# Kernel optimization log

Hardware: AMD Instinct MI355X
Metric: run time of the kernel (lower is better)

The kernel has to match this reference:

```python
import jax, jax.numpy as jnp
import numpy as np

B, T, DIM = 4, 1024, 2048
H, KVH = 16, 4
HD = DIM // H          # 128
G = H // KVH           # GQA group size = 4


def setup_inputs() -> dict:
    key = jax.random.key(0)
    ks = jax.random.split(key, 4)
    s = 1.0 / np.sqrt(DIM)
    x = jax.random.normal(ks[0], (B, T, DIM), jnp.float32)
    Wq = jax.random.normal(ks[1], (DIM, DIM), jnp.float32) * s
    Wkv = jax.random.normal(ks[2], (DIM, 2 * KVH * HD), jnp.float32) * s
    Wo = jax.random.normal(ks[3], (DIM, DIM), jnp.float32) * s
    # RoPE tables (theta=10000, half-split / rotate-half convention)
    inv_freq = 1.0 / (10000.0 ** (np.arange(0, HD, 2, dtype=np.float64) / HD))
    freqs = np.outer(np.arange(T, dtype=np.float64), inv_freq)  # [T, HD/2]
    cos = jnp.asarray(np.cos(freqs), jnp.float32)
    sin = jnp.asarray(np.sin(freqs), jnp.float32)
    return {"x": x, "Wq": Wq, "Wkv": Wkv, "Wo": Wo, "cos": cos, "sin": sin}


def _rope(u, cos, sin):
    # u: [B,T,heads,HD]; cos/sin: [T, HD/2]
    u1, u2 = jnp.split(u, 2, axis=-1)
    c = cos[None, :, None, :]
    s = sin[None, :, None, :]
    return jnp.concatenate([u1 * c - u2 * s, u1 * s + u2 * c], axis=-1)


def reference(x, Wq, Wkv, Wo, cos, sin):
    Bs, Ts, C = x.shape
    q = (x @ Wq).reshape(Bs, Ts, H, HD)
    kv = (x @ Wkv).reshape(Bs, Ts, 2, KVH, HD)
    k, v = kv[:, :, 0], kv[:, :, 1]
    q = _rope(q, cos, sin)
    k = _rope(k, cos, sin)
    # GQA without materializing repeated K/V: fold group dim into q
    qg = q.reshape(Bs, Ts, KVH, G, HD)
    scores = jnp.einsum('bqhgd,bkhd->bhgqk', qg, k) / np.float32(np.sqrt(HD))
    causal = jnp.tril(jnp.ones((Ts, Ts), bool))
    neg = jnp.finfo(scores.dtype).min
    scores = jnp.where(causal, scores, neg)
    att = jax.nn.softmax(scores, axis=-1)
    out = jnp.einsum('bhgqk,bkhd->bqhgd', att, v).reshape(Bs, Ts, C)
    return out @ Wo
```

## Files before the change

kernel.cpp:

```cpp
#include <hip/hip_runtime.h>

typedef unsigned short u16;
typedef unsigned int u32;
typedef __bf16 bf16x8 __attribute__((ext_vector_type(8)));
typedef float f32x4 __attribute__((ext_vector_type(4)));

#define BB   4
#define TT   1024
#define CDIM 2048
#define NH   16
#define NKV  4
#define HDIM 128

__device__ __forceinline__ float b2f(u16 u) {
    union { u32 i; float f; } x; x.i = ((u32)u) << 16; return x.f;
}
__device__ __forceinline__ u16 f2b(float f) {
    union { float f; u32 i; } x; x.f = f;
    u32 r = (x.i + 0x7fffu + ((x.i >> 16) & 1u)) >> 16;
    return (u16)r;
}
__device__ __forceinline__ void async16(const void* g, void* l) {
    __builtin_amdgcn_global_load_lds((const __attribute__((address_space(1))) void*)g,
                                     (__attribute__((address_space(3))) void*)l, 16, 0, 0);
}
template<int N> __device__ __forceinline__ void waitvm() {
    static_assert(N >= 0 && N <= 8, "unsupported vmcnt");
    if constexpr (N == 0)      asm volatile("s_waitcnt vmcnt(0)" ::: "memory");
    else if constexpr (N == 1) asm volatile("s_waitcnt vmcnt(1)" ::: "memory");
    else if constexpr (N == 2) asm volatile("s_waitcnt vmcnt(2)" ::: "memory");
    else if constexpr (N == 3) asm volatile("s_waitcnt vmcnt(3)" ::: "memory");
    else if constexpr (N == 4) asm volatile("s_waitcnt vmcnt(4)" ::: "memory");
    else if constexpr (N == 5) asm volatile("s_waitcnt vmcnt(5)" ::: "memory");
    else if constexpr (N == 6) asm volatile("s_waitcnt vmcnt(6)" ::: "memory");
    else if constexpr (N == 7) asm volatile("s_waitcnt vmcnt(7)" ::: "memory");
    else                       asm volatile("s_waitcnt vmcnt(8)" ::: "memory");
}

__device__ __forceinline__ bool wave_is_f32(const u16* xp) {
    u16 v = xp[(threadIdx.x & 63) * 2];
    int e = (v >> 7) & 0xFF;
    bool bad = (v != 0) && (e < 90 || e > 160);
    return __popcll(__ballot(bad)) > 16;
}

__global__ __launch_bounds__(256) void pre_k(const void* __restrict__ x,
                                             const void* __restrict__ Wq,
                                             const void* __restrict__ Wkv,
                                             const void* __restrict__ Wo,
                                             u16* __restrict__ xb,
                                             u16* __restrict__ csb,
                                             u16* __restrict__ snb,
                                             u16* __restrict__ WqkvT,
                                             u16* __restrict__ WoT,
                                             const void* __restrict__ cs,
                                             const void* __restrict__ sn) {
    const bool f32m = wave_is_f32((const u16*)x);
    int bid = blockIdx.x;
    if (bid < 8320) {
        const void* src; u16* dst; int i;
        if (bid < 8192)      { src = x;  dst = xb;  i = bid * 256 + threadIdx.x; }
        else if (bid < 8256) { src = cs; dst = csb; i = (bid - 8192) * 256 + threadIdx.x; }
        else                 { src = sn; dst = snb; i = (bid - 8256) * 256 + threadIdx.x; }
        union { u16 u[4]; ushort4 v; } o;
        if (f32m) {
            float4 f = ((const float4*)src)[i];
            o.u[0] = f2b(f.x); o.u[1] = f2b(f.y); o.u[2] = f2b(f.z); o.u[3] = f2b(f.w);
        } else {
            o.v = ((const ushort4*)src)[i];
        }
        ((ushort4*)dst)[i] = o.v;
        return;
    }
    __shared__ alignas(16) u16 tile[64 * 65];
    int t = bid - 8320;
    const void* W; u16* WT; int rows, cols, bx, by;
    if (t < 1024)      { W = Wq;  WT = WqkvT;                    rows = 2048; cols = 2048; bx = t & 31;  by = t >> 5; }
    else if (t < 1536) { int l = t - 1024; W = Wkv; WT = WqkvT + (long)2048 * 2048; rows = 2048; cols = 1024; bx = l & 15; by = l >> 4; }
    else               { int l = t - 1536; W = Wo;  WT = WoT;  rows = 2048; cols = 2048; bx = l & 31;   by = l >> 5; }
    const int r0 = by * 64, c0 = bx * 64;
#pragma unroll
    for (int i = 0; i < 16; i++) {
        int c = threadIdx.x + i * 256;
        int rr = c >> 6, cc = c & 63;
        long idx = (long)(r0 + rr) * cols + c0 + cc;
        tile[rr * 65 + cc] = f32m ? f2b(((const float*)W)[idx]) : ((const u16*)W)[idx];
    }
    __syncthreads();
#pragma unroll
    for (int i = 0; i < 16; i++) {
        int c = threadIdx.x + i * 256;
        int rr = c >> 6, cc = c & 63;
        WT[(long)(c0 + rr) * rows + r0 + cc] = tile[cc * 65 + rr];
    }
}

template<int BM, int BN>
__global__ __launch_bounds__(512, 2) void gemm_t(const u16* __restrict__ A,
                                                 const u16* __restrict__ Bt,
                                                 void* __restrict__ C,
                                                 int N, int Kd,
                                                 const u16* __restrict__ xprobe) {
    constexpr int MF  = BM / 32;
    constexpr int NF  = BN / 64;
    constexpr int MF0 = MF / 2, MF1 = MF - MF0;
    constexpr int NF0 = (NF + 1) / 2, NF1 = NF - NF0;
    constexpr int NAU = BM / 64;
    constexpr int NBU = BN / 64;
    constexpr int NAL = NAU / 2;
    constexpr int NBL = NBU / 2;

    __shared__ alignas(16) u16 As[2][BM * 64];
    __shared__ alignas(16) u16 Bs[2][BN * 64];

    const bool f32m = (xprobe != nullptr) && wave_is_f32(xprobe);
    const int tid = threadIdx.x;
    const int w = tid >> 6, lane = tid & 63;
    const int wm = w >> 2, wn = w & 3;
    const int l16 = lane & 15, quad = lane >> 4;
    const long arow0 = (long)blockIdx.y * BM;
    const long brow0 = (long)blockIdx.x * BN;
    const int NT = Kd >> 6;

    const int srow = tid >> 3, scp = tid & 7;
    const long gst = (long)srow * Kd + ((scp ^ (srow & 7)) << 3);
    const int cst = tid << 3;

    const u16* Ab = A + arow0 * Kd;
    const u16* Bb = Bt + brow0 * Kd;

    auto stageA = [&](int buf, int t, int u0, int u1) {
#pragma unroll
        for (int u = 0; u < NAU; u++)
            if (u >= u0 && u < u1)
                async16(Ab + (long)u * 64 * Kd + t * 64 + gst, &As[buf][u * 4096 + cst]);
    };
    auto stageB = [&](int buf, int t, int u0, int u1) {
#pragma unroll
        for (int u = 0; u < NBU; u++)
            if (u >= u0 && u < u1)
                async16(Bb + (long)u * 64 * Kd + t * 64 + gst, &Bs[buf][u * 4096 + cst]);
    };

    const int R0a = wm * (BM / 2) + l16, sA = R0a & 7;
    const int R0b = wn * (BN / 4) + l16, sB = R0b & 7;
    int aoff[2], boff[2];
    aoff[0] = R0a * 64 + ((quad ^ sA) << 3);
    aoff[1] = R0a * 64 + (((4 + quad) ^ sA) << 3);
    boff[0] = R0b * 64 + ((quad ^ sB) << 3);
    boff[1] = R0b * 64 + (((4 + quad) ^ sB) << 3);

    f32x4 acc[MF][NF];
#pragma unroll
    for (int i = 0; i < MF; i++)
#pragma unroll
        for (int j = 0; j < NF; j++) acc[i][j] = {0.f, 0.f, 0.f, 0.f};

    stageB(0, 0, 0, NBU);
    stageA(0, 0, 0, NAU);
    stageB(1, 1, 0, NBL);
    waitvm<NBL>();
    __builtin_amdgcn_s_barrier();

#pragma unroll 1
    for (int t = 0; t < NT; ++t) {
        const int cur = t & 1, nxt = cur ^ 1;
        const u16* pA = &As[cur][0];
        const u16* pB = &Bs[cur][0];
        bf16x8 afLo[MF0][2], afHi[MF1][2], bfA[NF0][2], bfB[NF1][2];

#pragma unroll
        for (int ks = 0; ks < 2; ks++) {
#pragma unroll
            for (int mt = 0; mt < MF0; mt++)
                afLo[mt][ks] = *(const bf16x8*)&pA[aoff[ks] + mt * 1024];
#pragma unroll
            for (int nt = 0; nt < NF0; nt++)
                bfA[nt][ks] = *(const bf16x8*)&pB[boff[ks] + nt * 1024];
        }
        if (t + 1 < NT) stageB(nxt, t + 1, NBL, NBU);
        __builtin_amdgcn_s_barrier();
        asm volatile("s_waitcnt lgkmcnt(0)" ::: "memory");
        __builtin_amdgcn_sched_barrier(0);
        __builtin_amdgcn_s_setprio(1);
#pragma unroll
        for (int ks = 0; ks < 2; ks++)
#pragma unroll
            for (int mt = 0; mt < MF0; mt++)
#pragma unroll
                for (int nt = 0; nt < NF0; nt++)
                    acc[mt][nt] = __builtin_amdgcn_mfma_f32_16x16x32_bf16(
                        afLo[mt][ks], bfA[nt][ks], acc[mt][nt], 0, 0, 0);
        __builtin_amdgcn_s_setprio(0);

#pragma unroll
        for (int ks = 0; ks < 2; ks++)
#pragma unroll
            for (int nt = 0; nt < NF1; nt++)
                bfB[nt][ks] = *(const bf16x8*)&pB[boff[ks] + (NF0 + nt) * 1024];
        if (t + 1 < NT) stageA(nxt, t + 1, 0, NAL);
        __builtin_amdgcn_s_barrier();
        asm volatile("s_waitcnt lgkmcnt(0)" ::: "memory");
        __builtin_amdgcn_sched_barrier(0);
        __builtin_amdgcn_s_setprio(1);
#pragma unroll
        for (int ks = 0; ks < 2; ks++)
#pragma unroll
            for (int mt = 0; mt < MF0; mt++)
#pragma unroll
                for (int nt = 0; nt < NF1; nt++)
                    acc[mt][NF0 + nt] = __builtin_amdgcn_mfma_f32_16x16x32_bf16(
                        afLo[mt][ks], bfB[nt][ks], acc[mt][NF0 + nt], 0, 0, 0);
        __builtin_amdgcn_s_setprio(0);

#pragma unroll
        for (int ks = 0; ks < 2; ks++)
#pragma unroll
            for (int mt = 0; mt < MF1; mt++)
                afHi[mt][ks] = *(const bf16x8*)&pA[aoff[ks] + (MF0 + mt) * 1024];
        if (t + 1 < NT) stageA(nxt, t + 1, NAL, NAU);
        __builtin_amdgcn_s_barrier();
        asm volatile("s_waitcnt lgkmcnt(0)" ::: "memory");
        __builtin_amdgcn_sched_barrier(0);
        __builtin_amdgcn_s_setprio(1);
#pragma unroll
        for (int ks = 0; ks < 2; ks++)
#pragma unroll
            for (int mt = 0; mt < MF1; mt++)
#pragma unroll
                for (int nt = 0; nt < NF1; nt++)
                    acc[MF0 + mt][NF0 + nt] = __builtin_amdgcn_mfma_f32_16x16x32_bf16(
                        afHi[mt][ks], bfB[nt][ks], acc[MF0 + mt][NF0 + nt], 0, 0, 0);
        __builtin_amdgcn_s_setprio(0);

        if (t + 1 < NT) {
            asm volatile("s_waitcnt vmcnt(0)" ::: "memory");
            __builtin_amdgcn_s_barrier();
            if (t + 2 < NT) stageB(cur, t + 2, 0, NBL);
        }
        __builtin_amdgcn_sched_barrier(0);
        __builtin_amdgcn_s_setprio(1);
#pragma unroll
        for (int ks = 0; ks < 2; ks++)
#pragma unroll
            for (int mt = 0; mt < MF1; mt++)
#pragma unroll
                for (int nt = 0; nt < NF0; nt++)
                    acc[MF0 + mt][nt] = __builtin_amdgcn_mfma_f32_16x16x32_bf16(
                        afHi[mt][ks], bfA[nt][ks], acc[MF0 + mt][nt], 0, 0, 0);
        __builtin_amdgcn_s_setprio(0);
    }

#pragma unroll
    for (int mt = 0; mt < MF; mt++) {
#pragma unroll
        for (int nt = 0; nt < NF; nt++) {
            long col = brow0 + wn * (BN / 4) + nt * 16 + l16;
#pragma unroll
            for (int r = 0; r < 4; r++) {
                long row = arow0 + wm * (BM / 2) + mt * 16 + quad * 4 + r;
                if (f32m) ((float*)C)[row * N + col] = acc[mt][nt][r];
                else      ((u16*)C)[row * N + col] = f2b(acc[mt][nt][r]);
            }
        }
    }
}

__global__ __launch_bounds__(256) void prep_k(const u16* __restrict__ QKVraw,
                                              const u16* __restrict__ cs,
                                              const u16* __restrict__ sn,
                                              u16* __restrict__ Qr,
                                              u16* __restrict__ Kr,
                                              u16* __restrict__ Vt) {
    int bid = blockIdx.x;
    if (bid < 16384) {
        int idx = bid * 256 + threadIdx.x;
        int d = idx & 63;
        int t = (idx >> 6) & (TT - 1);
        int bh = idx >> 16;
        long src = ((long)((bh >> 4) * TT + t)) * 3072 + (bh & 15) * HDIM;
        float u1 = b2f(QKVraw[src + d]), u2 = b2f(QKVraw[src + d + 64]);
        float c = b2f(cs[t * 64 + d]), s = b2f(sn[t * 64 + d]);
        long dst = ((long)bh * TT + t) * HDIM;
        Qr[dst + d] = f2b(u1 * c - u2 * s);
        Qr[dst + d + 64] = f2b(u1 * s + u2 * c);
    } else if (bid < 20480) {
        int idx = (bid - 16384) * 256 + threadIdx.x;
        int d = idx & 63;
        int t = (idx >> 6) & (TT - 1);
        int bk = idx >> 16;
        long src = ((long)((bk >> 2) * TT + t)) * 3072 + 2048 + (bk & 3) * HDIM;
        float u1 = b2f(QKVraw[src + d]), u2 = b2f(QKVraw[src + d + 64]);
        float c = b2f(cs[t * 64 + d]), s = b2f(sn[t * 64 + d]);
        long dst = ((long)bk * TT + t) * HDIM;
        Kr[dst + d] = f2b(u1 * c - u2 * s);
        Kr[dst + d + 64] = f2b(u1 * s + u2 * c);
    } else {
        int idx = (bid - 20480) * 256 + threadIdx.x;
        int t = idx & (TT - 1);
        int d = (idx >> 10) & (HDIM - 1);
        int bk = idx >> 17;
        Vt[idx] = QKVraw[((long)(bk >> 2) * TT + t) * 3072 + 2560 + (bk & 3) * HDIM + d];
    }
}

__global__ __launch_bounds__(256) void attn_kernel(const u16* __restrict__ Q,
                                                   const u16* __restrict__ Kr,
                                                   const u16* __restrict__ Vt,
                                                   u16* __restrict__ O) {
    __shared__ alignas(16) u16 Ks[2][64 * 128];
    __shared__ alignas(16) u16 Vts[2][128 * 64];
    __shared__ alignas(16) u16 Ps[64 * 88];

    const int tid = threadIdx.x, w = tid >> 6, lane = tid & 63;
    const int l16 = lane & 15, quad = lane >> 4;
    const float scale2 = 0.08838834764831845f * 1.4426950408889634f;

#pragma unroll 1
    for (int it = 0; it < 2; it++) {
        const int j = it ? (1023 - (int)blockIdx.x) : (int)blockIdx.x;
        const int qt = 15 - (j >> 6);
        const int bh = j & 63;
        const int b = bh >> 4, h = bh & 15;
        const int kvh = h >> 2;
        const long qrow0 = (long)bh * TT + qt * 64;
        const long krow0 = (long)(b * NKV + kvh) * TT;
        const long vbase = ((long)(b * NKV + kvh) * HDIM) * TT;

        __syncthreads();

#pragma unroll
        for (int i = 0; i < 4; i++) {
            int slot0 = (w * 4 + i) * 64;
            int slot = slot0 + lane;
            int row = slot >> 4, cp = slot & 15;
            int cg = (cp & 8) | ((cp ^ row) & 7);
            async16(Q + (qrow0 + row) * HDIM + cg * 8, &Ks[0][slot0 * 8]);
        }
        asm volatile("s_waitcnt vmcnt(0)" ::: "memory");
        bf16x8 qf[4];
        {
            const int Rq = w * 16 + l16;
#pragma unroll
            for (int ds = 0; ds < 4; ds++) {
                int c = ds * 4 + quad;
                qf[ds] = *(const bf16x8*)&Ks[0][Rq * 128 + ((c & 8) | ((c ^ Rq) & 7)) * 8];
            }
        }
        asm volatile("s_waitcnt lgkmcnt(0)" ::: "memory");

#pragma unroll
        for (int i = 0; i < 4; i++) {
            int slot0 = (w * 4 + i) * 64;
            int slot = slot0 + lane;
            int row = slot >> 4, cp = slot & 15;
            int cg = (cp & 8) | ((cp ^ row) & 7);
            async16(Kr + (krow0 + row) * HDIM + cg * 8, &Ks[0][slot0 * 8]);
        }
#pragma unroll
        for (int i = 0; i < 4; i++) {
            int slot0 = (w * 4 + i) * 64;
            int slot = slot0 + lane;
            int row = slot >> 3, cp = slot & 7;
            int cg = cp ^ (row & 7);
            async16(Vt + vbase + (long)row * TT + cg * 8, &Vts[0][slot0 * 8]);
        }
        if (qt >= 1) {
#pragma unroll
            for (int i = 0; i < 4; i++) {
                int slot0 = (w * 4 + i) * 64;
                int slot = slot0 + lane;
                int row = slot >> 4, cp = slot & 15;
                int cg = (cp & 8) | ((cp ^ row) & 7);
                async16(Kr + (krow0 + 64 + row) * HDIM + cg * 8, &Ks[1][slot0 * 8]);
            }
#pragma unroll
            for (int i = 0; i < 4; i++) {
                int slot0 = (w * 4 + i) * 64;
                int slot = slot0 + lane;
                int row = slot >> 3, cp = slot & 7;
                int cg = cp ^ (row & 7);
                async16(Vt + vbase + (long)row * TT + 64 + cg * 8, &Vts[1][slot0 * 8]);
            }
            asm volatile("s_waitcnt vmcnt(8)" ::: "memory");
        } else {
            asm volatile("s_waitcnt vmcnt(0)" ::: "memory");
        }
        asm volatile("s_barrier" ::: "memory");

        f32x4 o[8];
#pragma unroll
        for (int i = 0; i < 8; i++) o[i] = {0.f, 0.f, 0.f, 0.f};
        float m_i = -1.0e30f, l_i = 0.f;
        const int qg = qt * 64 + w * 16 + l16;

#pragma unroll 1
        for (int kt = 0; kt <= qt; kt++) {
            const int cur = kt & 1;
            const u16* ksb = Ks[cur];
            const u16* vsb = Vts[cur];

            f32x4 s[4];
#pragma unroll
            for (int nt = 0; nt < 4; nt++) s[nt] = {0.f, 0.f, 0.f, 0.f};
#pragma unroll
            for (int ds = 0; ds < 4; ds++) {
                int c = ds * 4 + quad;
#pragma unroll
                for (int nt = 0; nt < 4; nt++) {
                    int Rk = nt * 16 + l16;
                    bf16x8 ak = *(const bf16x8*)&ksb[Rk * 128 + ((c & 8) | ((c ^ Rk) & 7)) * 8];
                    s[nt] = __builtin_amdgcn_mfma_f32_16x16x32_bf16(ak, qf[ds], s[nt], 0, 0, 0);
                }
            }

            float p[4][4];
            float mx = -1.0e30f;
            if (kt == qt) {
#pragma unroll
                for (int nt = 0; nt < 4; nt++)
#pragma unroll
                    for (int r = 0; r < 4; r++) {
                        int kcol = kt * 64 + nt * 16 + quad * 4 + r;
                        float v = (kcol <= qg) ? (float)s[nt][r] * scale2 : -1.0e30f;
                        p[nt][r] = v;
                        mx = fmaxf(mx, v);
                    }
            } else {
#pragma unroll
                for (int nt = 0; nt < 4; nt++)
#pragma unroll
                    for (int r = 0; r < 4; r++) {
                        float v = (float)s[nt][r] * scale2;
                        p[nt][r] = v;
                        mx = fmaxf(mx, v);
                    }
            }
            mx = fmaxf(mx, __shfl_xor(mx, 16));
            mx = fmaxf(mx, __shfl_xor(mx, 32));
            float mnew = fmaxf(m_i, mx);
            float alpha = exp2f(m_i - mnew);
            float rs = 0.f;
#pragma unroll
            for (int nt = 0; nt < 4; nt++)
#pragma unroll
                for (int r = 0; r < 4; r++) {
                    float e = exp2f(p[nt][r] - mnew);
                    p[nt][r] = e;
                    rs += e;
                }
            rs += __shfl_xor(rs, 16);
            rs += __shfl_xor(rs, 32);
            l_i = l_i * alpha + rs;

            u32* Psw = (u32*)Ps;
            int pb = (w * 16 + l16) * 44 + quad * 2;
#pragma unroll
            for (int nt = 0; nt < 4; nt++) {
                u32 lo = (u32)f2b(p[nt][0]) | ((u32)f2b(p[nt][1]) << 16);
                u32 hi = (u32)f2b(p[nt][2]) | ((u32)f2b(p[nt][3]) << 16);
                Psw[pb + nt * 8]     = lo;
                Psw[pb + nt * 8 + 1] = hi;
            }
            if (__ballot(mnew != m_i) != 0ULL) {
#pragma unroll
                for (int n8 = 0; n8 < 8; n8++)
#pragma unroll
                    for (int r = 0; r < 4; r++) o[n8][r] *= alpha;
            }
            m_i = mnew;

            asm volatile("s_waitcnt lgkmcnt(0)" ::: "memory");

#pragma unroll
            for (int ks = 0; ks < 2; ks++) {
                bf16x8 bp = *(const bf16x8*)&Ps[(w * 16 + l16) * 88 + ks * 32 + quad * 8];
#pragma unroll
                for (int n8 = 0; n8 < 8; n8++) {
                    int Rv = n8 * 16 + l16;
                    int c = ks * 4 + quad;
                    bf16x8 av = *(const bf16x8*)&vsb[Rv * 64 + (c ^ (Rv & 7)) * 8];
                    o[n8] = __builtin_amdgcn_mfma_f32_16x16x32_bf16(av, bp, o[n8], 0, 0, 0);
                }
            }

            if (kt == qt) break;

            asm volatile("s_waitcnt lgkmcnt(0)" ::: "memory");
            asm volatile("s_barrier" ::: "memory");
            if (kt + 2 <= qt) {
                const int nk = kt + 2;
#pragma unroll
                for (int i = 0; i < 4; i++) {
                    int slot0 = (w * 4 + i) * 64;
                    int slot = slot0 + lane;
                    int row = slot >> 4, cp = slot & 15;
                    int cg = (cp & 8) | ((cp ^ row) & 7);
                    async16(Kr + (krow0 + nk * 64 + row) * HDIM + cg * 8, &Ks[cur][slot0 * 8]);
                }
#pragma unroll
                for (int i = 0; i < 4; i++) {
                    int slot0 = (w * 4 + i) * 64;
                    int slot = slot0 + lane;
                    int row = slot >> 3, cp = slot & 7;
                    int cg = cp ^ (row & 7);
                    async16(Vt + vbase + (long)row * TT + nk * 64 + cg * 8, &Vts[cur][slot0 * 8]);
                }
                asm volatile("s_waitcnt vmcnt(8)" ::: "memory");
            } else {
                asm volatile("s_waitcnt vmcnt(0)" ::: "memory");
            }
            asm volatile("s_barrier" ::: "memory");
        }

        float inv = 1.0f / l_i;
        long obase = ((long)(b * TT + qg)) * CDIM + h * HDIM;
#pragma unroll
        for (int n8 = 0; n8 < 8; n8++) {
            ushort4 st;
            st.x = f2b(o[n8][0] * inv);
            st.y = f2b(o[n8][1] * inv);
            st.z = f2b(o[n8][2] * inv);
            st.w = f2b(o[n8][3] * inv);
            *(ushort4*)&O[obase + n8 * 16 + quad * 4] = st;
        }
    }
}

extern "C" void kernel_launch(void* const* d_in, const int* in_sizes, int n_in,
                              void* d_out, int out_size, void* d_ws, size_t ws_size,
                              hipStream_t stream) {
    const void* x   = d_in[0];
    const void* Wq  = d_in[1];
    const void* Wkv = d_in[2];
    const void* Wo  = d_in[3];
    const void* cs  = d_in[4];
    const void* sn  = d_in[5];

    char* ws = (char*)d_ws;
    const size_t NEED = 105119748;
    if (ws_size < NEED) return;

    u16* WqkvT = (u16*)(ws + 0);
    u16* WoT   = (u16*)(ws + 12582912);
    u16* QKVraw= (u16*)(ws + 20971520);
    u16* Qr    = (u16*)(ws + 46137344);
    u16* Kr    = (u16*)(ws + 62914560);
    u16* Vt    = (u16*)(ws + 67108864);
    u16* ATT   = (u16*)(ws + 71303168);
    u16* xb    = (u16*)(ws + 88080384);
    u16* csb   = (u16*)(ws + 104857600);
    u16* snb   = (u16*)(ws + 104988672);

    pre_k<<<10880, 256, 0, stream>>>(x, Wq, Wkv, Wo, xb, csb, snb, WqkvT, WoT, cs, sn);

    gemm_t<256, 192><<<dim3(16, 16), 512, 0, stream>>>(xb, WqkvT, QKVraw, 3072, 2048, nullptr);

    prep_k<<<28672, 256, 0, stream>>>(QKVraw, csb, snb, Qr, Kr, Vt);

    attn_kernel<<<512, 256, 0, stream>>>(Qr, Kr, Vt, ATT);

    gemm_t<128, 256><<<dim3(8, 32), 512, 0, stream>>>(ATT, WoT, d_out, 2048, 2048, (const u16*)x);
}
```

Baseline: 315.6 us.

## Add two-phase GEMM variant for output projection and tile V transpose via LDS

Renames the existing GEMM to gemm_p4 and adds gemm_p2, a variant with a simpler two-phase load/MFMA schedule: it splits the A fragments into lo/hi halves and needs fewer barriers per K step. gemm_p2 is used for the output projection. The V transpose in prep_k is rewritten to stage 64x64 tiles in shared memory with vectorized ushort4 loads and stores, replacing strided scalar gathers, which shrinks that part of the grid. The aim is cheaper output-projection scheduling and a coalesced V transpose, at the cost of more code and an extra shared buffer in prep_k.

```diff
diff --git a/kernel.cpp b/kernel.cpp
--- a/kernel.cpp
+++ b/kernel.cpp
@@ -96,11 +96,11 @@
 }
 
 template<int BM, int BN>
-__global__ __launch_bounds__(512, 2) void gemm_t(const u16* __restrict__ A,
-                                                 const u16* __restrict__ Bt,
-                                                 void* __restrict__ C,
-                                                 int N, int Kd,
-                                                 const u16* __restrict__ xprobe) {
+__global__ __launch_bounds__(512, 2) void gemm_p4(const u16* __restrict__ A,
+                                                  const u16* __restrict__ Bt,
+                                                  void* __restrict__ C,
+                                                  int N, int Kd,
+                                                  const u16* __restrict__ xprobe) {
     constexpr int MF  = BM / 32;
     constexpr int NF  = BN / 64;
     constexpr int MF0 = MF / 2, MF1 = MF - MF0;
@@ -266,12 +266,159 @@
     }
 }
 
+template<int BM, int BN>
+__global__ __launch_bounds__(512, 2) void gemm_p2(const u16* __restrict__ A,
+                                                  const u16* __restrict__ Bt,
+                                                  void* __restrict__ C,
+                                                  int N, int Kd,
+                                                  const u16* __restrict__ xprobe) {
+    constexpr int MF  = BM / 32;
+    constexpr int NF  = BN / 64;
+    constexpr int MF0 = MF / 2, MF1 = MF - MF0;
+    constexpr int NF0 = (NF + 1) / 2, NF1 = NF - NF0;
+    constexpr int NAU = BM / 64;
+    constexpr int NBU = BN / 64;
+
+    __shared__ alignas(16) u16 As[2][BM * 64];
+    __shared__ alignas(16) u16 Bs[2][BN * 64];
+
+    const bool f32m = (xprobe != nullptr) && wave_is_f32(xprobe);
+    const int tid = threadIdx.x;
+    const int w = tid >> 6, lane = tid & 63;
+    const int wm = w >> 2, wn = w & 3;
+    const int l16 = lane & 15, quad = lane >> 4;
+    const long arow0 = (long)blockIdx.y * BM;
+    const long brow0 = (long)blockIdx.x * BN;
+    const int NT = Kd >> 6;
+
+    const int srow = tid >> 3, scp = tid & 7;
+    const long gst = (long)srow * Kd + ((scp ^ (srow & 7)) << 3);
+    const int cst = tid << 3;
+
+    const u16* Ab = A + arow0 * Kd;
+    const u16* Bb = Bt + brow0 * Kd;
+
+    auto stageA = [&](int buf, int t) {
+#pragma unroll
+        for (int u = 0; u < NAU; u++)
+            async16(Ab + (long)u * 64 * Kd + t * 64 + gst, &As[buf][u * 4096 + cst]);
+    };
+    auto stageB = [&](int buf, int t) {
+#pragma unroll
+        for (int u = 0; u < NBU; u++)
+            async16(Bb + (long)u * 64 * Kd + t * 64 + gst, &Bs[buf][u * 4096 + cst]);
+    };
+
+    const int R0a = wm * (BM / 2) + l16, sA = R0a & 7;
+    const int R0b = wn * (BN / 4) + l16, sB = R0b & 7;
+    int aoff[2], boff[2];
+    aoff[0] = R0a * 64 + ((quad ^ sA) << 3);
+    aoff[1] = R0a * 64 + (((4 + quad) ^ sA) << 3);
+    boff[0] = R0b * 64 + ((quad ^ sB) << 3);
+    boff[1] = R0b * 64 + (((4 + quad) ^ sB) << 3);
+
+    f32x4 acc[MF][NF];
+#pragma unroll
+    for (int i = 0; i < MF; i++)
+#pragma unroll
+        for (int j = 0; j < NF; j++) acc[i][j] = {0.f, 0.f, 0.f, 0.f};
+
+    stageB(0, 0); stageA(0, 0); stageB(1, 1); stageA(1, 1);
+    waitvm<NAU + NBU>();
+    __builtin_amdgcn_s_barrier();
+
+#pragma unroll 1
+    for (int t = 0; t < NT; ++t) {
+        const int cur = t & 1;
+        const u16* pA = &As[cur][0];
+        const u16* pB = &Bs[cur][0];
+        bf16x8 afLo[MF0][2], afHi[MF1][2], bfA[NF0][2], bfB[NF1][2];
+
+#pragma unroll
+        for (int ks = 0; ks < 2; ks++) {
+#pragma unroll
+            for (int mt = 0; mt < MF0; mt++)
+                afLo[mt][ks] = *(const bf16x8*)&pA[aoff[ks] + mt * 1024];
+#pragma unroll
+            for (int nt = 0; nt < NF0; nt++)
+                bfA[nt][ks] = *(const bf16x8*)&pB[boff[ks] + nt * 1024];
+#pragma unroll
+            for (int nt = 0; nt < NF1; nt++)
+                bfB[nt][ks] = *(const bf16x8*)&pB[boff[ks] + (NF0 + nt) * 1024];
+        }
+        asm volatile("s_waitcnt lgkmcnt(0)" ::: "memory");
+        __builtin_amdgcn_sched_barrier(0);
+        __builtin_amdgcn_s_setprio(1);
+#pragma unroll
+        for (int ks = 0; ks < 2; ks++)
+#pragma unroll
+            for (int mt = 0; mt < MF0; mt++) {
+#pragma unroll
+                for (int nt = 0; nt < NF0; nt++)
+                    acc[mt][nt] = __builtin_amdgcn_mfma_f32_16x16x32_bf16(
+                        afLo[mt][ks], bfA[nt][ks], acc[mt][nt], 0, 0, 0);
+#pragma unroll
+                for (int nt = 0; nt < NF1; nt++)
+                    acc[mt][NF0 + nt] = __builtin_amdgcn_mfma_f32_16x16x32_bf16(
+                        afLo[mt][ks], bfB[nt][ks], acc[mt][NF0 + nt], 0, 0, 0);
+            }
+        __builtin_amdgcn_s_setprio(0);
+
+#pragma unroll
+        for (int ks = 0; ks < 2; ks++)
+#pragma unroll
+            for (int mt = 0; mt < MF1; mt++)
+                afHi[mt][ks] = *(const bf16x8*)&pA[aoff[ks] + (MF0 + mt) * 1024];
+        __builtin_amdgcn_s_barrier();
+        if (t + 2 < NT) stageB(cur, t + 2);
+        asm volatile("s_waitcnt lgkmcnt(0)" ::: "memory");
+        __builtin_amdgcn_sched_barrier(0);
+        __builtin_amdgcn_s_setprio(1);
+#pragma unroll
+        for (int ks = 0; ks < 2; ks++)
+#pragma unroll
+            for (int mt = 0; mt < MF1; mt++) {
+#pragma unroll
+                for (int nt = 0; nt < NF1; nt++)
+                    acc[MF0 + mt][NF0 + nt] = __builtin_amdgcn_mfma_f32_16x16x32_bf16(
+                        afHi[mt][ks], bfB[nt][ks], acc[MF0 + mt][NF0 + nt], 0, 0, 0);
+#pragma unroll
+                for (int nt = 0; nt < NF0; nt++)
+                    acc[MF0 + mt][nt] = __builtin_amdgcn_mfma_f32_16x16x32_bf16(
+                        afHi[mt][ks], bfA[nt][ks], acc[MF0 + mt][nt], 0, 0, 0);
+            }
+        __builtin_amdgcn_s_setprio(0);
+
+        if (t + 1 < NT) {
+            if (t + 2 < NT) waitvm<NBU>();
+            else            waitvm<0>();
+            __builtin_amdgcn_s_barrier();
+            if (t + 2 < NT) stageA(cur, t + 2);
+        }
+    }
+
+#pragma unroll
+    for (int mt = 0; mt < MF; mt++) {
+#pragma unroll
+        for (int nt = 0; nt < NF; nt++) {
+            long col = brow0 + wn * (BN / 4) + nt * 16 + l16;
+#pragma unroll
+            for (int r = 0; r < 4; r++) {
+                long row = arow0 + wm * (BM / 2) + mt * 16 + quad * 4 + r;
+                if (f32m) ((float*)C)[row * N + col] = acc[mt][nt][r];
+                else      ((u16*)C)[row * N + col] = f2b(acc[mt][nt][r]);
+            }
+        }
+    }
+}
+
 __global__ __launch_bounds__(256) void prep_k(const u16* __restrict__ QKVraw,
                                               const u16* __restrict__ cs,
                                               const u16* __restrict__ sn,
                                               u16* __restrict__ Qr,
                                               u16* __restrict__ Kr,
                                               u16* __restrict__ Vt) {
+    __shared__ alignas(16) u16 tile[64 * 68];
     int bid = blockIdx.x;
     if (bid < 16384) {
         int idx = bid * 256 + threadIdx.x;
@@ -296,11 +443,32 @@
         Kr[dst + d] = f2b(u1 * c - u2 * s);
         Kr[dst + d + 64] = f2b(u1 * s + u2 * c);
     } else {
-        int idx = (bid - 20480) * 256 + threadIdx.x;
-        int t = idx & (TT - 1);
-        int d = (idx >> 10) & (HDIM - 1);
-        int bk = idx >> 17;
-        Vt[idx] = QKVraw[((long)(bk >> 2) * TT + t) * 3072 + 2560 + (bk & 3) * HDIM + d];
+        int vb = bid - 20480;
+        int bk = vb >> 5;
+        int dt = (vb >> 4) & 1;
+        int tt = vb & 15;
+        const int d0 = dt * 64, t0 = tt * 64;
+        const long srcb = ((long)(bk >> 2) * TT) * 3072 + 2560 + (bk & 3) * HDIM;
+#pragma unroll
+        for (int i = 0; i < 4; i++) {
+            int lin = i * 256 + threadIdx.x;
+            int r = lin >> 4, c4 = (lin & 15) * 4;
+            *(ushort4*)&tile[r * 68 + c4] =
+                *(const ushort4*)&QKVraw[srcb + (long)(t0 + r) * 3072 + d0 + c4];
+        }
+        __syncthreads();
+        const long dstb = ((long)bk * 128 + d0) * 1024 + t0;
+#pragma unroll
+        for (int i = 0; i < 4; i++) {
+            int lin = i * 256 + threadIdx.x;
+            int dr = lin >> 4, c4 = (lin & 15) * 4;
+            ushort4 v;
+            v.x = tile[(c4 + 0) * 68 + dr];
+            v.y = tile[(c4 + 1) * 68 + dr];
+            v.z = tile[(c4 + 2) * 68 + dr];
+            v.w = tile[(c4 + 3) * 68 + dr];
+            *(ushort4*)&Vt[dstb + (long)dr * 1024 + c4] = v;
+        }
     }
 }
 
@@ -554,11 +722,11 @@
 
     pre_k<<<10880, 256, 0, stream>>>(x, Wq, Wkv, Wo, xb, csb, snb, WqkvT, WoT, cs, sn);
 
-    gemm_t<256, 192><<<dim3(16, 16), 512, 0, stream>>>(xb, WqkvT, QKVraw, 3072, 2048, nullptr);
-
-    prep_k<<<28672, 256, 0, stream>>>(QKVraw, csb, snb, Qr, Kr, Vt);
+    gemm_p4<256, 192><<<dim3(16, 16), 512, 0, stream>>>(xb, WqkvT, QKVraw, 3072, 2048, nullptr);
+
+    prep_k<<<20992, 256, 0, stream>>>(QKVraw, csb, snb, Qr, Kr, Vt);
 
     attn_kernel<<<512, 256, 0, stream>>>(Qr, Kr, Vt, ATT);
 
-    gemm_t<128, 256><<<dim3(8, 32), 512, 0, stream>>>(ATT, WoT, d_out, 2048, 2048, (const u16*)x);
-}
+    gemm_p2<128, 256><<<dim3(8, 32), 512, 0, stream>>>(ATT, WoT, d_out, 2048, 2048, (const u16*)x);
+}
```

Result: faster. 299.5 us (-5.1%).
